# Kernel optimization log

Measured on AMD Instinct MI355X. Metric: run time of the kernel, lower is better.

The kernel has to match this reference:

```python
import jax, jax.numpy as jnp
import numpy as np

# Module hyperparameters (init_kwargs)
FS = 30.0          # sampling rate (Hz)
HIGH_PASS = 40.0   # bpm
LOW_PASS = 250.0   # bpm
DELTA_T = 300      # crop length (samples)
K = 64             # crops per (batch, channel)
B, C, T = 256, 16, 9000

NBINS = DELTA_T // 2 + 1  # rfft bins
# freqs = linspace(0, Fs/2, NBINS); band mask is static given shapes
_freqs = np.linspace(0.0, FS / 2.0, NBINS)
MASK_IDX = np.where((_freqs >= HIGH_PASS / 60.0) & (_freqs <= LOW_PASS / 60.0))[0]


def setup_inputs() -> dict:
    key = jax.random.key(0)
    k1, k2 = jax.random.split(key)
    inp = jax.random.normal(k1, (B, C, T), dtype=jnp.float32)
    # random temporal offsets, one per (b, c, k) crop
    offsets = jax.random.randint(k2, (B, C, K), 0, T - DELTA_T + 1, dtype=jnp.int32)
    return {"input": inp, "offsets": offsets}


def reference(input, offsets):
    # Batched gather of all random crops: [B, C, K, DELTA_T]
    t_idx = offsets[..., None] + jnp.arange(DELTA_T, dtype=jnp.int32)  # [B,C,K,dt]
    crops = jnp.take_along_axis(input[:, :, None, :], t_idx, axis=-1)
    # Remove per-crop mean
    crops = crops - jnp.mean(crops, axis=-1, keepdims=True)
    # rFFT with 'forward' norm (divide by n), power spectrum
    spec = jnp.fft.rfft(crops, axis=-1, norm='forward')   # [B,C,K,NBINS] complex
    power = spec.real ** 2 + spec.imag ** 2               # [B,C,K,NBINS]
    # Keep only the heart-rate band (static index set), normalize to unit sum
    power = power[..., MASK_IDX]                          # [B,C,K,F_band]
    power = power / jnp.sum(power, axis=-1, keepdims=True)
    return power
```

## Files before the change

kernel.cpp:

```cpp
#include <hip/hip_runtime.h>
#include <math.h>

#define TT 9000
#define DT 300
#define KK 64
#define NB 35
#define KMIN 7
#define NCH 4096
#define NPAIR (KK * NB)


typedef __bf16 bf16;
typedef __attribute__((ext_vector_type(8))) __bf16 bf16x8;
typedef __attribute__((ext_vector_type(4))) __bf16 bf16x4;
typedef __attribute__((ext_vector_type(4))) float f32x4;

#define NFRAG_ELEMS (10 * 6 * 64 * 8)
#define WBYTES 61440

__global__ void build_w(bf16* __restrict__ tab) {
    int i = blockIdx.x * blockDim.x + threadIdx.x;
    if (i >= NFRAG_ELEMS) return;
    int j    = i & 7;
    int l    = (i >> 3) & 63;
    int f    = i >> 9;
    int nt   = f % 6;
    int ks   = f / 6;
    int quad = l >> 4;
    int c    = l & 15;
    int k    = ks * 32 + quad * 8 + j;
    int jf   = (nt % 3) * 16 + c;
    float v = 0.0f;
    if (jf <= NB - 1 && k < DT) {
        int bin = jf + KMIN;
        int ph  = (bin * k) % DT;
        float ang = 0.02094395102393195f * (float)ph;
        v = (nt >= 3) ? sinf(ang) : cosf(ang);
    }
    tab[i] = (bf16)v;
}

#define SPAD 9024

__global__ __launch_bounds__(768, 6) void st_mfma(
        const float* __restrict__ input,
        const int*   __restrict__ offsets,
        const bf16*  __restrict__ tab,
        float*       __restrict__ out) {
    __shared__ __align__(16) bf16 sig[SPAD];
    __shared__ __align__(16) unsigned char wlds[WBYTES];
    __shared__ __align__(16) float part[KK][3];
    __shared__ int offs[KK];

    const int bc   = blockIdx.x;
    const int tid  = threadIdx.x;
    const int wid  = tid >> 6;
    const int lane = tid & 63;

#pragma unroll
    for (int i = 0; i < 5; ++i) {
        int chunk = wid * 5 + i;
        __builtin_amdgcn_global_load_lds(
            (const __attribute__((address_space(1))) void*)((const unsigned char*)tab + chunk * 1024 + lane * 16),
            (__attribute__((address_space(3))) void*)(wlds + chunk * 1024),
            16, 0, 0);
    }

    const float4* src = (const float4*)(input + (size_t)bc * TT);
#pragma unroll
    for (int i = 0; i < 3; ++i) {
        int idx = tid + i * 768;
        if (idx < TT / 4) {
            float4 v = src[idx];
            bf16x4 b;
            b[0] = (bf16)v.x; b[1] = (bf16)v.y; b[2] = (bf16)v.z; b[3] = (bf16)v.w;
            *(bf16x4*)(sig + idx * 4) = b;
        }
    }
    if (tid < SPAD - TT) sig[TT + tid] = (bf16)0.0f;
    if (tid < KK) offs[tid] = offsets[bc * KK + tid];
    __syncthreads();

    const int m    = wid & 3;
    const int pg   = wid >> 2;
    const int quad = lane >> 4;
    const int c    = lane & 15;

    const int off = offs[m * 16 + c];
    const int d0  = (off + quad * 8) >> 1;
    const unsigned sh = (unsigned)((off & 1) << 4);
    const int* ip = (const int*)sig;

    const unsigned char* wp = wlds + (size_t)(pg * 64 + lane) * 16;

    f32x4 acc_c = {0.f,0.f,0.f,0.f}, acc_s = {0.f,0.f,0.f,0.f};

#pragma unroll
    for (int ks = 0; ks < 10; ++ks) {
        const int db = d0 + ks * 16;
        int dw0 = ip[db + 0], dw1 = ip[db + 1], dw2 = ip[db + 2],
            dw3 = ip[db + 3], dw4 = ip[db + 4];
        union { unsigned u[4]; bf16x8 v; } a;
        a.u[0] = __builtin_amdgcn_alignbit((unsigned)dw1, (unsigned)dw0, sh);
        a.u[1] = __builtin_amdgcn_alignbit((unsigned)dw2, (unsigned)dw1, sh);
        a.u[2] = __builtin_amdgcn_alignbit((unsigned)dw3, (unsigned)dw2, sh);
        a.u[3] = __builtin_amdgcn_alignbit((unsigned)dw4, (unsigned)dw3, sh);

        bf16x8 wc = *(const bf16x8*)(wp + (ks * 6    ) * 1024);
        bf16x8 wn = *(const bf16x8*)(wp + (ks * 6 + 3) * 1024);
        acc_c = __builtin_amdgcn_mfma_f32_16x16x32_bf16(a.v, wc, acc_c, 0, 0, 0);
        acc_s = __builtin_amdgcn_mfma_f32_16x16x32_bf16(a.v, wn, acc_s, 0, 0, 0);
    }

    float pv[4];
#pragma unroll
    for (int r = 0; r < 4; ++r) {
        float p = acc_c[r] * acc_c[r] + acc_s[r] * acc_s[r];
        pv[r] = p;
        float s = p;
#pragma unroll
        for (int d = 1; d < 16; d <<= 1) s += __shfl_xor(s, d, 64);
        if (c == 0) part[m * 16 + quad * 4 + r][pg] = s;
    }
    __syncthreads();

    float* ob = out + (size_t)bc * NPAIR;
#pragma unroll
    for (int r = 0; r < 4; ++r) {
        int crop = m * 16 + quad * 4 + r;
        float s = part[crop][0] + part[crop][1] + part[crop][2];
        float rinv = __builtin_amdgcn_rcpf(s);
        if (pg < 2 || c < 3)
            ob[crop * NB + pg * 16 + c] = pv[r] * rinv;
    }
}

extern "C" void kernel_launch(void* const* d_in, const int* in_sizes, int n_in,
                              void* d_out, int out_size, void* d_ws, size_t ws_size,
                              hipStream_t stream) {
    const float* input   = (const float*)d_in[0];
    const int*   offsets = (const int*)d_in[1];
    float*       out     = (float*)d_out;
    bf16*        tab     = (bf16*)d_ws;

    build_w<<<(NFRAG_ELEMS + 255) / 256, 256, 0, stream>>>(tab);
    st_mfma<<<NCH, 768, 0, stream>>>(input, offsets, tab, out);
}
```

Baseline: 233.2 us.

## Batch channels per block with warp-specialized double-buffered crop gather

```diff
diff --git a/kernel.cpp b/kernel.cpp
--- a/kernel.cpp
+++ b/kernel.cpp
@@ -40,98 +40,109 @@
     tab[i] = (bf16)v;
 }
 
-#define SPAD 9024
+#define ROWB 656
+#define CBB  (KK * ROWB)
+#define CPB  8
+#define NBLK (NCH / CPB)
 
-__global__ __launch_bounds__(768, 6) void st_mfma(
+__device__ __forceinline__ void gather_ch(const float* __restrict__ chan,
+                                          const int* __restrict__ offp,
+                                          unsigned char* __restrict__ dst,
+                                          int t, int nthreads, int niter) {
+#pragma unroll
+    for (int i = 0; i < niter; ++i) {
+        int n = t + i * nthreads;
+        int r = n / 80;
+        int p = n - r * 80;
+        float f0 = 0.f, f1 = 0.f, f2 = 0.f, f3 = 0.f;
+        if (p < 75) {
+            const float* gp = chan + offp[r] + p * 4;
+            f0 = gp[0]; f1 = gp[1]; f2 = gp[2]; f3 = gp[3];
+        }
+        bf16x4 v;
+        v[0] = (bf16)f0; v[1] = (bf16)f1; v[2] = (bf16)f2; v[3] = (bf16)f3;
+        *(bf16x4*)(dst + r * ROWB + p * 8) = v;
+    }
+}
+
+__global__ __launch_bounds__(1024, 4) void st_mfma(
         const float* __restrict__ input,
         const int*   __restrict__ offsets,
         const bf16*  __restrict__ tab,
         float*       __restrict__ out) {
-    __shared__ __align__(16) bf16 sig[SPAD];
     __shared__ __align__(16) unsigned char wlds[WBYTES];
+    __shared__ __align__(16) unsigned char cb[2][CBB];
     __shared__ __align__(16) float part[KK][3];
-    __shared__ int offs[KK];
 
     const int bc   = blockIdx.x;
     const int tid  = threadIdx.x;
     const int wid  = tid >> 6;
     const int lane = tid & 63;
+    const int ch0  = bc * CPB;
 
+    if (wid < 15) {
 #pragma unroll
-    for (int i = 0; i < 5; ++i) {
-        int chunk = wid * 5 + i;
-        __builtin_amdgcn_global_load_lds(
-            (const __attribute__((address_space(1))) void*)((const unsigned char*)tab + chunk * 1024 + lane * 16),
-            (__attribute__((address_space(3))) void*)(wlds + chunk * 1024),
-            16, 0, 0);
-    }
-
-    const float4* src = (const float4*)(input + (size_t)bc * TT);
-#pragma unroll
-    for (int i = 0; i < 3; ++i) {
-        int idx = tid + i * 768;
-        if (idx < TT / 4) {
-            float4 v = src[idx];
-            bf16x4 b;
-            b[0] = (bf16)v.x; b[1] = (bf16)v.y; b[2] = (bf16)v.z; b[3] = (bf16)v.w;
-            *(bf16x4*)(sig + idx * 4) = b;
+        for (int i = 0; i < 4; ++i) {
+            int chunk = wid * 4 + i;
+            __builtin_amdgcn_global_load_lds(
+                (const __attribute__((address_space(1))) void*)((const unsigned char*)tab + chunk * 1024 + lane * 16),
+                (__attribute__((address_space(3))) void*)(wlds + chunk * 1024),
+                16, 0, 0);
         }
     }
-    if (tid < SPAD - TT) sig[TT + tid] = (bf16)0.0f;
-    if (tid < KK) offs[tid] = offsets[bc * KK + tid];
-    __syncthreads();
+    gather_ch(input + (size_t)ch0 * TT, offsets + (size_t)ch0 * KK,
+              cb[0], tid, 1024, 5);
 
     const int m    = wid & 3;
     const int pg   = wid >> 2;
     const int quad = lane >> 4;
     const int c    = lane & 15;
+    const unsigned char* wbase = wlds + pg * 1024 + lane * 16;
+    const int arow = (m * 16 + c) * ROWB + quad * 16;
 
-    const int off = offs[m * 16 + c];
-    const int d0  = (off + quad * 8) >> 1;
-    const unsigned sh = (unsigned)((off & 1) << 4);
-    const int* ip = (const int*)sig;
+    for (int ch = 0; ch < CPB; ++ch) {
+        __syncthreads();
 
-    const unsigned char* wp = wlds + (size_t)(pg * 64 + lane) * 16;
+        if (wid < 12) {
+            const unsigned char* ab = cb[ch & 1] + arow;
+            f32x4 acc_c = {0.f,0.f,0.f,0.f}, acc_s = {0.f,0.f,0.f,0.f};
+#pragma unroll
+            for (int ks = 0; ks < 10; ++ks) {
+                bf16x8 a  = *(const bf16x8*)(ab + ks * 64);
+                bf16x8 wc = *(const bf16x8*)(wbase + ks * 6144);
+                bf16x8 wn = *(const bf16x8*)(wbase + ks * 6144 + 3072);
+                acc_c = __builtin_amdgcn_mfma_f32_16x16x32_bf16(a, wc, acc_c, 0, 0, 0);
+                acc_s = __builtin_amdgcn_mfma_f32_16x16x32_bf16(a, wn, acc_s, 0, 0, 0);
+            }
+            float pv[4];
+#pragma unroll
+            for (int r = 0; r < 4; ++r) {
+                float p = acc_c[r] * acc_c[r] + acc_s[r] * acc_s[r];
+                pv[r] = p;
+                float s = p;
+#pragma unroll
+                for (int d = 1; d < 16; d <<= 1) s += __shfl_xor(s, d, 64);
+                if (c == 0) part[m * 16 + quad * 4 + r][pg] = s;
+            }
+            __syncthreads();
 
-    f32x4 acc_c = {0.f,0.f,0.f,0.f}, acc_s = {0.f,0.f,0.f,0.f};
-
+            float* ob = out + (size_t)(ch0 + ch) * NPAIR;
 #pragma unroll
-    for (int ks = 0; ks < 10; ++ks) {
-        const int db = d0 + ks * 16;
-        int dw0 = ip[db + 0], dw1 = ip[db + 1], dw2 = ip[db + 2],
-            dw3 = ip[db + 3], dw4 = ip[db + 4];
-        union { unsigned u[4]; bf16x8 v; } a;
-        a.u[0] = __builtin_amdgcn_alignbit((unsigned)dw1, (unsigned)dw0, sh);
-        a.u[1] = __builtin_amdgcn_alignbit((unsigned)dw2, (unsigned)dw1, sh);
-        a.u[2] = __builtin_amdgcn_alignbit((unsigned)dw3, (unsigned)dw2, sh);
-        a.u[3] = __builtin_amdgcn_alignbit((unsigned)dw4, (unsigned)dw3, sh);
-
-        bf16x8 wc = *(const bf16x8*)(wp + (ks * 6    ) * 1024);
-        bf16x8 wn = *(const bf16x8*)(wp + (ks * 6 + 3) * 1024);
-        acc_c = __builtin_amdgcn_mfma_f32_16x16x32_bf16(a.v, wc, acc_c, 0, 0, 0);
-        acc_s = __builtin_amdgcn_mfma_f32_16x16x32_bf16(a.v, wn, acc_s, 0, 0, 0);
-    }
-
-    float pv[4];
-#pragma unroll
-    for (int r = 0; r < 4; ++r) {
-        float p = acc_c[r] * acc_c[r] + acc_s[r] * acc_s[r];
-        pv[r] = p;
-        float s = p;
-#pragma unroll
-        for (int d = 1; d < 16; d <<= 1) s += __shfl_xor(s, d, 64);
-        if (c == 0) part[m * 16 + quad * 4 + r][pg] = s;
-    }
-    __syncthreads();
-
-    float* ob = out + (size_t)bc * NPAIR;
-#pragma unroll
-    for (int r = 0; r < 4; ++r) {
-        int crop = m * 16 + quad * 4 + r;
-        float s = part[crop][0] + part[crop][1] + part[crop][2];
-        float rinv = __builtin_amdgcn_rcpf(s);
-        if (pg < 2 || c < 3)
-            ob[crop * NB + pg * 16 + c] = pv[r] * rinv;
+            for (int r = 0; r < 4; ++r) {
+                int crop = m * 16 + quad * 4 + r;
+                float s = part[crop][0] + part[crop][1] + part[crop][2];
+                float rinv = __builtin_amdgcn_rcpf(s);
+                if (pg < 2 || c < 3)
+                    ob[crop * NB + pg * 16 + c] = pv[r] * rinv;
+            }
+        } else {
+            if (ch + 1 < CPB) {
+                int chn = ch0 + ch + 1;
+                gather_ch(input + (size_t)chn * TT, offsets + (size_t)chn * KK,
+                          cb[(ch + 1) & 1], tid - 768, 256, 20);
+            }
+            __syncthreads();
+        }
     }
 }
 
@@ -144,5 +155,5 @@
     bf16*        tab     = (bf16*)d_ws;
 
     build_w<<<(NFRAG_ELEMS + 255) / 256, 256, 0, stream>>>(tab);
-    st_mfma<<<NCH, 768, 0, stream>>>(input, offsets, tab, out);
+    st_mfma<<<NBLK, 1024, 0, stream>>>(input, offsets, tab, out);
 }
```

Result: slower. 406.4 us (+74.3%).
